# Kernel optimization log

Measured on AMD Instinct MI355X. Metric: run time of the kernel, lower is better.

Reference implementation:

```python
import jax, jax.numpy as jnp
import numpy as np

B, D, R, T = 128, 256, 128, 128  # batch, hidden_dim, num_regions, seq_length


def setup_inputs() -> dict:
    key = jax.random.key(0)
    ks = jax.random.split(key, 16)
    s = 0.02
    inp = {
        "h": jax.random.normal(ks[0], (B, D), dtype=jnp.float32),
        # Linear weights stored as [in, out] (y = x @ W + b), transpose of torch layout
        "Wq": jax.random.normal(ks[1], (D, D), dtype=jnp.float32) * s,
        "bq": jnp.zeros((D,), jnp.float32),
        "Wk": jax.random.normal(ks[2], (D, D), dtype=jnp.float32) * s,
        "bk": jnp.zeros((D,), jnp.float32),
        "Wc": jax.random.normal(ks[3], (D * D, D), dtype=jnp.float32) * s,  # context_proj
        "bc": jnp.zeros((D,), jnp.float32),
        "Wa": jax.random.normal(ks[4], (D, R), dtype=jnp.float32) * s,      # action_proj
        "ba": jnp.zeros((R,), jnp.float32),
        # GRUCell params, torch layout: weight_ih [3D, D] (r|z|n), weight_hh [3D, D]
        "W_ih": jax.random.normal(ks[5], (3 * D, D), dtype=jnp.float32) * s,
        "W_hh": jax.random.normal(ks[6], (3 * D, D), dtype=jnp.float32) * s,
        "b_ih": jnp.zeros((3 * D,), jnp.float32),
        "b_hh": jnp.zeros((3 * D,), jnp.float32),
    }
    return inp


def _forward(h, Wq, bq, Wk, bk, Wc, bc, Wa, ba, W_ih, W_hh, b_ih, b_hh):
    query = h @ Wq + bq                      # [B, D]
    key_v = h @ Wk + bk                      # [B, D]

    # context = bmm(query[:, :, None], key[:, None, :]) is identical every step
    # (query/key are loop-invariant), so compute context_embed once and broadcast.
    context = query[:, :, None] * key_v[:, None, :]          # [B, D, D]
    context_embed = context.reshape(B, D * D) @ Wc + bc      # [B, D]
    s_list = jnp.broadcast_to(context_embed[:, None, :], (B, T, D))

    # GRU input is the loop-invariant key -> precompute input gates once.
    x_gates = key_v @ W_ih.T + b_ih                          # [B, 3D]
    xr, xz, xn = jnp.split(x_gates, 3, axis=-1)

    region_ids = jnp.arange(R)

    def step(carry, _):
        hidden, used = carry                                  # [B,D], [B,R] bool
        logits = hidden @ Wa + ba                             # [B, R]
        masked = jnp.where(used, -jnp.inf, logits)
        # argmax(softmax(masked)) == argmax(masked)
        action = jnp.argmax(masked, axis=-1)                  # [B]
        used_new = used | (region_ids[None, :] == action[:, None])
        # GRUCell(key, hidden)
        h_gates = hidden @ W_hh.T + b_hh
        hr, hz, hn = jnp.split(h_gates, 3, axis=-1)
        r = jax.nn.sigmoid(xr + hr)
        z = jax.nn.sigmoid(xz + hz)
        n = jnp.tanh(xn + r * hn)
        hidden_new = (1.0 - z) * n + z * hidden
        return (hidden_new, used_new), (action, masked, hidden)

    used0 = jnp.zeros((B, R), dtype=bool)
    _, (actions, mask_scores, h_traj) = jax.lax.scan(step, (h, used0), None, length=T)

    actions = actions.T                                       # [B, T]
    mask_scores = jnp.transpose(mask_scores, (1, 0, 2))       # [B, T, R]
    h_list = jnp.transpose(h_traj, (1, 0, 2))                 # [B, T, D]
    c_list = h_list                                           # c_list appends same tensor
    return actions, mask_scores, s_list, h_list, c_list


def reference(h, Wq, bq, Wk, bk, Wc, bc, Wa, ba, W_ih, W_hh, b_ih, b_hh):
    return _forward(h, Wq, bq, Wk, bk, Wc, bc, Wa, ba, W_ih, W_hh, b_ih, b_hh)
```

## Files before the change

### kernel.cpp

```cpp
#include <hip/hip_runtime.h>
#include <math.h>

#define BB 128
#define DD 256
#define RR 128
#define TT 128
#define G3 768

#define DREG 64
#define DLDS 48
#define DSTR 144

#define MASKED_SENTINEL -3.0e38f

__global__ __launch_bounds__(256) void k_prep(
    const float* __restrict__ h,
    const float* __restrict__ Wq, const float* __restrict__ bq,
    const float* __restrict__ Wk, const float* __restrict__ bk,
    float* __restrict__ q, float* __restrict__ k)
{
    __shared__ float hl[DD];
    const int b = blockIdx.x, t = threadIdx.x;
    hl[t] = h[b * DD + t];
    __syncthreads();
    float aq = bq[t], ak = bk[t];
#pragma unroll 8
    for (int d = 0; d < DD; ++d) {
        const float hd = hl[d];
        aq = fmaf(hd, Wq[d * DD + t], aq);
        ak = fmaf(hd, Wk[d * DD + t], ak);
    }
    q[b * DD + t] = aq;
    k[b * DD + t] = ak;
}

__global__ __launch_bounds__(1024) void k_transpose(
    const float* __restrict__ W_hh, const float* __restrict__ W_ih,
    float4* __restrict__ Wt4, float* __restrict__ Wih_t)
{
    const int e = blockIdx.x * 1024 + threadIdx.x;
    if (e < 64 * G3) {
        const int i4 = e / G3, g = e % G3;
        Wt4[e] = *(const float4*)&W_hh[(size_t)g * DD + 4 * i4];
    } else {
        const int e2 = e - 64 * G3;
        const int d = e2 / G3, g = e2 % G3;
        Wih_t[e2] = W_ih[(size_t)g * DD + d];
    }
}

__global__ __launch_bounds__(512) void k_ctx1(
    const float* __restrict__ q, const float* __restrict__ k,
    const float* __restrict__ Wc, float* __restrict__ partial)
{
    __shared__ float kl[32][257];
    const int i = blockIdx.x >> 2, b0 = (blockIdx.x & 3) * 32;
    const int o = threadIdx.x & 255, ph = threadIdx.x >> 8;
    const float* __restrict__ Wci = Wc + (size_t)i * DD * DD;

    for (int r = ph; r < 32; r += 2) kl[r][o] = k[(b0 + r) * DD + o];
    __syncthreads();

    const int bb0 = ph * 16;
    float acc[16];
#pragma unroll
    for (int bb = 0; bb < 16; ++bb) acc[bb] = 0.f;
#pragma unroll 4
    for (int j = 0; j < DD; ++j) {
        const float w = Wci[j * DD + o];
#pragma unroll
        for (int bb = 0; bb < 16; ++bb)
            acc[bb] = fmaf(kl[bb0 + bb][j], w, acc[bb]);
    }
#pragma unroll
    for (int bb = 0; bb < 16; ++bb)
        partial[((size_t)i * BB + (b0 + bb0 + bb)) * DD + o] =
            acc[bb] * q[(b0 + bb0 + bb) * DD + i];
}

__global__ __launch_bounds__(256) void k_ctx2(
    const float* __restrict__ partial, const float* __restrict__ bc,
    float* __restrict__ s_out)
{
    const int b = blockIdx.x, o = threadIdx.x;
    float s = bc[o];
#pragma unroll 8
    for (int i = 0; i < DD; ++i)
        s += partial[((size_t)i * BB + b) * DD + o];
    float* __restrict__ dst = s_out + (size_t)b * TT * DD + o;
#pragma unroll 4
    for (int t = 0; t < TT; ++t) dst[(size_t)t * DD] = s;
}

__global__ __launch_bounds__(768) void k_gru(
    const float* __restrict__ h0, const float* __restrict__ kv_g,
    const float* __restrict__ b_ih, const float* __restrict__ b_hh,
    const float4* __restrict__ Wt4, const float* __restrict__ Wih_t,
    float* __restrict__ out_h, float* __restrict__ out_c)
{
    __shared__ __align__(16) float hid[DD];
    __shared__ float xg[G3];
    __shared__ float hg[G3];
    __shared__ float lw[DLDS * G3];

    const int b = blockIdx.x, t = threadIdx.x;

    if (t < DD) hid[t] = h0[b * DD + t];

    float4 wr[16];
#pragma unroll
    for (int c = 0; c < 16; ++c) wr[c] = Wt4[c * G3 + t];

    for (int c = 0; c < 12; ++c) {
        const float4 w = Wt4[(16 + c) * G3 + t];
        lw[(4 * c + 0) * G3 + t] = w.x;
        lw[(4 * c + 1) * G3 + t] = w.y;
        lw[(4 * c + 2) * G3 + t] = w.z;
        lw[(4 * c + 3) * G3 + t] = w.w;
    }

    {
        const float* __restrict__ kvp = kv_g + b * DD;
        float s0 = 0.f, s1 = 0.f, s2 = 0.f, s3 = 0.f;
#pragma unroll 2
        for (int d = 0; d < DD; d += 4) {
            s0 = fmaf(kvp[d + 0], Wih_t[(size_t)(d + 0) * G3 + t], s0);
            s1 = fmaf(kvp[d + 1], Wih_t[(size_t)(d + 1) * G3 + t], s1);
            s2 = fmaf(kvp[d + 2], Wih_t[(size_t)(d + 2) * G3 + t], s2);
            s3 = fmaf(kvp[d + 3], Wih_t[(size_t)(d + 3) * G3 + t], s3);
        }
        xg[t] = b_ih[t] + ((s0 + s1) + (s2 + s3));
    }
    const float bias = b_hh[t];
    const float4* __restrict__ wstr = Wt4 + (size_t)28 * G3 + t;
    __syncthreads();

    for (int step = 0; step < TT; ++step) {
        if (t < 256)      out_h[((size_t)b * TT + step) * DD + t] = hid[t];
        else if (t < 512) out_c[((size_t)b * TT + step) * DD + (t - 256)] = hid[t - 256];

        float a0 = 0.f, a1 = 0.f, a2 = 0.f, a3 = 0.f;
#pragma unroll
        for (int c = 0; c < 16; ++c) {
            const float4 hv = *(const float4*)&hid[4 * c];
            a0 = fmaf(hv.x, wr[c].x, a0);
            a1 = fmaf(hv.y, wr[c].y, a1);
            a2 = fmaf(hv.z, wr[c].z, a2);
            a3 = fmaf(hv.w, wr[c].w, a3);
        }
#pragma unroll 8
        for (int dd = 0; dd < DLDS; ++dd) {
            const float w = lw[dd * G3 + t];
            const float hv = hid[DREG + dd];
            if ((dd & 3) == 0)      a0 = fmaf(hv, w, a0);
            else if ((dd & 3) == 1) a1 = fmaf(hv, w, a1);
            else if ((dd & 3) == 2) a2 = fmaf(hv, w, a2);
            else                    a3 = fmaf(hv, w, a3);
        }
#pragma unroll 6
        for (int c = 0; c < 36; ++c) {
            const float4 w = wstr[(size_t)c * G3];
            const float4 hv = *(const float4*)&hid[DREG + DLDS + 4 * c];
            a0 = fmaf(hv.x, w.x, a0);
            a1 = fmaf(hv.y, w.y, a1);
            a2 = fmaf(hv.z, w.z, a2);
            a3 = fmaf(hv.w, w.w, a3);
        }
        hg[t] = ((a0 + a1) + (a2 + a3)) + bias;
        __syncthreads();

        if (t < DD) {
            const int d = t;
            const float old = hid[d];
            const float rr = 1.f / (1.f + expf(-(xg[d] + hg[d])));
            const float zz = 1.f / (1.f + expf(-(xg[DD + d] + hg[DD + d])));
            const float nn = tanhf(xg[2 * DD + d] + rr * hg[2 * DD + d]);
            hid[d] = (1.f - zz) * nn + zz * old;
        }
        __syncthreads();
    }
}

__global__ __launch_bounds__(256) void k_logits(
    const float* __restrict__ h_list, const float* __restrict__ Wa,
    const float* __restrict__ ba, float* __restrict__ out_mask)
{
    __shared__ float hl[16][DD];
    const int bt0 = blockIdx.x * 16;
    const int t = threadIdx.x, r = t & 127, g = t >> 7;

#pragma unroll
    for (int j = 0; j < 16; ++j)
        hl[j][t] = h_list[(size_t)(bt0 + j) * DD + t];
    __syncthreads();

    float acc[8];
#pragma unroll
    for (int j = 0; j < 8; ++j) acc[j] = 0.f;
#pragma unroll 4
    for (int d = 0; d < DD; ++d) {
        const float w = Wa[(size_t)d * RR + r];
#pragma unroll
        for (int j = 0; j < 8; ++j)
            acc[j] = fmaf(hl[g * 8 + j][d], w, acc[j]);
    }
    const float bar = ba[r];
#pragma unroll
    for (int j = 0; j < 8; ++j)
        out_mask[(size_t)(bt0 + g * 8 + j) * RR + r] = acc[j] + bar;
}

__global__ __launch_bounds__(128) void k_scan(
    float* __restrict__ mask, float* __restrict__ out_act)
{
    __shared__ float lg[TT * RR];
    const int b = blockIdx.x, t = threadIdx.x;
    float4* __restrict__ mb4 = (float4*)(mask + (size_t)b * TT * RR);

    for (int c = t; c < TT * RR / 4; c += 128)
        ((float4*)lg)[c] = mb4[c];
    __syncthreads();

    if (t < 64) {
        bool u0 = false, u1 = false;
        for (int t2 = 0; t2 < TT; ++t2) {
            const float l0 = lg[t2 * RR + t];
            const float l1 = lg[t2 * RR + 64 + t];
            lg[t2 * RR + t]      = u0 ? MASKED_SENTINEL : l0;
            lg[t2 * RR + 64 + t] = u1 ? MASKED_SENTINEL : l1;
            float v1 = u0 ? -INFINITY : l0;  int i1 = t;
            const float m1 = u1 ? -INFINITY : l1;
            if (m1 > v1) { v1 = m1; i1 = t + 64; }
#pragma unroll
            for (int off = 32; off > 0; off >>= 1) {
                const float ov = __shfl_down(v1, off);
                const int   oi = __shfl_down(i1, off);
                if (ov > v1 || (ov == v1 && oi < i1)) { v1 = ov; i1 = oi; }
            }
            const int win = __shfl(i1, 0);
            if (t == 0) out_act[(size_t)b * TT + t2] = (float)win;
            u0 = u0 || (win == t);
            u1 = u1 || (win == t + 64);
        }
    }
    __syncthreads();

    for (int c = t; c < TT * RR / 4; c += 128)
        mb4[c] = ((float4*)lg)[c];
}

extern "C" void kernel_launch(void* const* d_in, const int* in_sizes, int n_in,
                              void* d_out, int out_size, void* d_ws, size_t ws_size,
                              hipStream_t stream) {
    const float* h    = (const float*)d_in[0];
    const float* Wq   = (const float*)d_in[1];
    const float* bq   = (const float*)d_in[2];
    const float* Wk   = (const float*)d_in[3];
    const float* bk   = (const float*)d_in[4];
    const float* Wc   = (const float*)d_in[5];
    const float* bc   = (const float*)d_in[6];
    const float* Wa   = (const float*)d_in[7];
    const float* ba   = (const float*)d_in[8];
    const float* W_ih = (const float*)d_in[9];
    const float* W_hh = (const float*)d_in[10];
    const float* b_ih = (const float*)d_in[11];
    const float* b_hh = (const float*)d_in[12];

    float* out = (float*)d_out;
    float* out_act  = out;
    float* out_mask = out + 16384;
    float* out_s    = out + 16384 + 2097152;
    float* out_h    = out + 16384 + 2097152 + 4194304;
    float* out_c    = out_h + 4194304;

    float*  q     = (float*)d_ws;
    float*  k     = q + BB * DD;
    float4* Wt4   = (float4*)(k + BB * DD);
    float*  Wih_t = (float*)(Wt4 + 64 * G3);
    float* partial = out_h;

    k_transpose<<<240, 1024, 0, stream>>>(W_hh, W_ih, Wt4, Wih_t);
    k_prep<<<BB, 256, 0, stream>>>(h, Wq, bq, Wk, bk, q, k);
    k_ctx1<<<1024, 512, 0, stream>>>(q, k, Wc, partial);
    k_ctx2<<<BB, 256, 0, stream>>>(partial, bc, out_s);
    k_gru<<<BB, 768, 0, stream>>>(h, k, b_ih, b_hh, Wt4, Wih_t, out_h, out_c);
    k_logits<<<1024, 256, 0, stream>>>(out_h, Wa, ba, out_mask);
    k_scan<<<BB, 128, 0, stream>>>(out_mask, out_act);
}
```

Measured before the change: 894.8 us.

## Tile transposes via LDS, accumulate ctx partials in-block, fold s_list writes into GRU

```diff
diff --git a/kernel.cpp b/kernel.cpp
--- a/kernel.cpp
+++ b/kernel.cpp
@@ -34,18 +34,46 @@
     k[b * DD + t] = ak;
 }
 
-__global__ __launch_bounds__(1024) void k_transpose(
+__global__ __launch_bounds__(512) void k_transpose(
     const float* __restrict__ W_hh, const float* __restrict__ W_ih,
     float4* __restrict__ Wt4, float* __restrict__ Wih_t)
 {
-    const int e = blockIdx.x * 1024 + threadIdx.x;
-    if (e < 64 * G3) {
-        const int i4 = e / G3, g = e % G3;
-        Wt4[e] = *(const float4*)&W_hh[(size_t)g * DD + 4 * i4];
+    const int t = threadIdx.x;
+    if (blockIdx.x < 12) {
+        __shared__ float4 ld4[64][65];
+        const int g0 = blockIdx.x * 64;
+        const float4* __restrict__ in4 = (const float4*)W_hh;
+#pragma unroll
+        for (int c = 0; c < 8; ++c) {
+            const int idx = c * 512 + t;
+            const int row = idx >> 6, col = idx & 63;
+            ld4[row][col] = in4[(size_t)(g0 + row) * 64 + col];
+        }
+        __syncthreads();
+#pragma unroll
+        for (int c = 0; c < 8; ++c) {
+            const int idx = c * 512 + t;
+            const int i4 = idx >> 6, gg = idx & 63;
+            Wt4[(size_t)i4 * G3 + g0 + gg] = ld4[gg][i4];
+        }
     } else {
-        const int e2 = e - 64 * G3;
-        const int d = e2 / G3, g = e2 % G3;
-        Wih_t[e2] = W_ih[(size_t)g * DD + d];
+        __shared__ float lds[64][65];
+        const int bb = blockIdx.x - 12;
+        const int g0 = (bb >> 2) * 64;
+        const int d0 = (bb & 3) * 64;
+#pragma unroll
+        for (int c = 0; c < 8; ++c) {
+            const int idx = c * 512 + t;
+            const int row = idx >> 6, col = idx & 63;
+            lds[row][col] = W_ih[(size_t)(g0 + row) * DD + d0 + col];
+        }
+        __syncthreads();
+#pragma unroll
+        for (int c = 0; c < 8; ++c) {
+            const int idx = c * 512 + t;
+            const int dd = idx >> 6, gg = idx & 63;
+            Wih_t[(size_t)(d0 + dd) * G3 + g0 + gg] = lds[gg][dd];
+        }
     }
 }
 
@@ -54,49 +82,58 @@
     const float* __restrict__ Wc, float* __restrict__ partial)
 {
     __shared__ float kl[32][257];
-    const int i = blockIdx.x >> 2, b0 = (blockIdx.x & 3) * 32;
+    const int ig = blockIdx.x >> 2, b0 = (blockIdx.x & 3) * 32;
     const int o = threadIdx.x & 255, ph = threadIdx.x >> 8;
-    const float* __restrict__ Wci = Wc + (size_t)i * DD * DD;
 
     for (int r = ph; r < 32; r += 2) kl[r][o] = k[(b0 + r) * DD + o];
     __syncthreads();
 
     const int bb0 = ph * 16;
-    float acc[16];
-#pragma unroll
-    for (int bb = 0; bb < 16; ++bb) acc[bb] = 0.f;
+    float tot[16];
+#pragma unroll
+    for (int bb = 0; bb < 16; ++bb) tot[bb] = 0.f;
+
+    for (int ii = 0; ii < 4; ++ii) {
+        const int i = ig * 4 + ii;
+        const float* __restrict__ Wci = Wc + (size_t)i * DD * DD;
+        float acc[16];
+#pragma unroll
+        for (int bb = 0; bb < 16; ++bb) acc[bb] = 0.f;
 #pragma unroll 4
-    for (int j = 0; j < DD; ++j) {
-        const float w = Wci[j * DD + o];
+        for (int j = 0; j < DD; ++j) {
+            const float w = Wci[j * DD + o];
+#pragma unroll
+            for (int bb = 0; bb < 16; ++bb)
+                acc[bb] = fmaf(kl[bb0 + bb][j], w, acc[bb]);
+        }
 #pragma unroll
         for (int bb = 0; bb < 16; ++bb)
-            acc[bb] = fmaf(kl[bb0 + bb][j], w, acc[bb]);
+            tot[bb] = fmaf(acc[bb], q[(b0 + bb0 + bb) * DD + i], tot[bb]);
     }
 #pragma unroll
     for (int bb = 0; bb < 16; ++bb)
-        partial[((size_t)i * BB + (b0 + bb0 + bb)) * DD + o] =
-            acc[bb] * q[(b0 + bb0 + bb) * DD + i];
-}
-
-__global__ __launch_bounds__(256) void k_ctx2(
+        partial[((size_t)ig * BB + (b0 + bb0 + bb)) * DD + o] = tot[bb];
+}
+
+__global__ __launch_bounds__(256) void k_ctx2red(
     const float* __restrict__ partial, const float* __restrict__ bc,
-    float* __restrict__ s_out)
+    float* __restrict__ ce)
 {
     const int b = blockIdx.x, o = threadIdx.x;
     float s = bc[o];
 #pragma unroll 8
-    for (int i = 0; i < DD; ++i)
-        s += partial[((size_t)i * BB + b) * DD + o];
-    float* __restrict__ dst = s_out + (size_t)b * TT * DD + o;
-#pragma unroll 4
-    for (int t = 0; t < TT; ++t) dst[(size_t)t * DD] = s;
+    for (int g = 0; g < 64; ++g)
+        s += partial[((size_t)g * BB + b) * DD + o];
+    ce[b * DD + o] = s;
 }
 
 __global__ __launch_bounds__(768) void k_gru(
     const float* __restrict__ h0, const float* __restrict__ kv_g,
     const float* __restrict__ b_ih, const float* __restrict__ b_hh,
     const float4* __restrict__ Wt4, const float* __restrict__ Wih_t,
-    float* __restrict__ out_h, float* __restrict__ out_c)
+    const float* __restrict__ ce,
+    float* __restrict__ out_h, float* __restrict__ out_c,
+    float* __restrict__ out_s)
 {
     __shared__ __align__(16) float hid[DD];
     __shared__ float xg[G3];
@@ -106,6 +143,7 @@
     const int b = blockIdx.x, t = threadIdx.x;
 
     if (t < DD) hid[t] = h0[b * DD + t];
+    const float ce_reg = (t >= 512) ? ce[b * DD + (t - 512)] : 0.f;
 
     float4 wr[16];
 #pragma unroll
@@ -138,6 +176,7 @@
     for (int step = 0; step < TT; ++step) {
         if (t < 256)      out_h[((size_t)b * TT + step) * DD + t] = hid[t];
         else if (t < 512) out_c[((size_t)b * TT + step) * DD + (t - 256)] = hid[t - 256];
+        else              out_s[((size_t)b * TT + step) * DD + (t - 512)] = ce_reg;
 
         float a0 = 0.f, a1 = 0.f, a2 = 0.f, a3 = 0.f;
 #pragma unroll
@@ -277,13 +316,15 @@
     float*  k     = q + BB * DD;
     float4* Wt4   = (float4*)(k + BB * DD);
     float*  Wih_t = (float*)(Wt4 + 64 * G3);
+    float*  ce    = Wih_t + DD * G3;
     float* partial = out_h;
 
-    k_transpose<<<240, 1024, 0, stream>>>(W_hh, W_ih, Wt4, Wih_t);
+    k_transpose<<<60, 512, 0, stream>>>(W_hh, W_ih, Wt4, Wih_t);
     k_prep<<<BB, 256, 0, stream>>>(h, Wq, bq, Wk, bk, q, k);
-    k_ctx1<<<1024, 512, 0, stream>>>(q, k, Wc, partial);
-    k_ctx2<<<BB, 256, 0, stream>>>(partial, bc, out_s);
-    k_gru<<<BB, 768, 0, stream>>>(h, k, b_ih, b_hh, Wt4, Wih_t, out_h, out_c);
+    k_ctx1<<<256, 512, 0, stream>>>(q, k, Wc, partial);
+    k_ctx2red<<<BB, 256, 0, stream>>>(partial, bc, ce);
+    k_gru<<<BB, 768, 0, stream>>>(h, k, b_ih, b_hh, Wt4, Wih_t, ce,
+                                  out_h, out_c, out_s);
     k_logits<<<1024, 256, 0, stream>>>(out_h, Wa, ba, out_mask);
     k_scan<<<BB, 128, 0, stream>>>(out_mask, out_act);
 }
```

New measurement: 1.033 ms. 1.15x slower.
